# Performance work log

Measured on AMD Instinct MI355X. Metric: run time of the kernel, lower is better.

## Reference

```python
import jax
jax.config.update("jax_enable_x64", True)
import jax.numpy as jnp
import numpy as np

N = 20000      # nodes per batched graph
E = 320000     # random edges (avg degree 16)
F = 128        # input node features
EMB = 128      # embedding_size
H = 3          # num_heads
G = 128        # graphs in batch (for AvgPooling)
NEG_SLOPE = 0.2  # DGL GATConv attention LeakyReLU slope


def setup_inputs():
    key = jax.random.key(0)
    ks = jax.random.split(key, 40)

    def rn(k, shape):
        return jax.random.normal(k, shape, jnp.float32) * 0.1

    inp = {}
    inp["featsA"] = jax.random.normal(ks[0], (N, F), jnp.float32)
    inp["featsB"] = jax.random.normal(ks[1], (N, F), jnp.float32)
    # edges: random + self-loops so every node has >=1 incoming edge
    for nm, ka, kb in (("A", ks[2], ks[3]), ("B", ks[4], ks[5])):
        src = jnp.concatenate([jax.random.randint(ka, (E,), 0, N, jnp.int32),
                               jnp.arange(N, dtype=jnp.int32)])
        dst = jnp.concatenate([jax.random.randint(kb, (E,), 0, N, jnp.int32),
                               jnp.arange(N, dtype=jnp.int32)])
        inp["src" + nm] = src
        inp["dst" + nm] = dst
        inp["gid" + nm] = ((jnp.arange(N) * G) // N).astype(jnp.int32)

    # per-branch parameters (two independent GATNet_1 branches)
    i = 6
    for nm in ("A", "B"):
        inp["W1" + nm] = rn(ks[i], (F, H * EMB)); i += 1      # gat1A fc
        inp["al1" + nm] = rn(ks[i], (H, EMB)); i += 1          # attn_l
        inp["ar1" + nm] = rn(ks[i], (H, EMB)); i += 1          # attn_r
        inp["b1" + nm] = rn(ks[i], (H * EMB,)); i += 1         # bias
        inp["Wn" + nm] = rn(ks[i], (EMB, H * EMB)); i += 1     # gatn fc
        inp["aln" + nm] = rn(ks[i], (H, EMB)); i += 1
        inp["arn" + nm] = rn(ks[i], (H, EMB)); i += 1
        inp["bn" + nm] = rn(ks[i], (H * EMB,)); i += 1
        inp["Wl" + nm] = rn(ks[i], (H * EMB, EMB)); i += 1     # linear1A
        inp["bl" + nm] = rn(ks[i], (EMB,)); i += 1
    inp["Wo"] = rn(ks[i], (2 * EMB, 1)); i += 1                # DoubleNet.output
    inp["bo"] = rn(ks[i], (1,))
    return inp


def gat_layer(feat, src, dst, W, al, ar, b):
    # DGL GATConv (eval mode: feat_drop/attn_drop are identity)
    n = feat.shape[0]
    z = (feat @ W).reshape(n, H, -1)                     # [N,H,D]
    el = (z * al[None]).sum(-1)                          # [N,H]
    er = (z * ar[None]).sum(-1)
    e = jax.nn.leaky_relu(el[src] + er[dst], NEG_SLOPE)  # [E,H]
    # edge softmax over incoming edges of each dst node
    m = jax.ops.segment_max(e, dst, num_segments=n)
    a = jnp.exp(e - m[dst])
    den = jax.ops.segment_sum(a, dst, num_segments=n)
    a = a / den[dst]
    out = jax.ops.segment_sum(a[:, :, None] * z[src], dst, num_segments=n)  # [N,H,D]
    return out + b.reshape(1, H, -1)


def branch(feat, src, dst, gid, W1, al1, ar1, b1, Wn, aln, arn, bn, Wl, bl):
    n = feat.shape[0]
    x = gat_layer(feat, src, dst, W1, al1, ar1, b1).reshape(n, -1)
    x = x @ Wl + bl
    for _ in range(2):  # two applications of the SAME gatn/linear1A weights
        x = gat_layer(x, src, dst, Wn, aln, arn, bn).reshape(n, -1)
        x = x @ Wl + bl
        # nn.LeakyReLU(True): negative_slope == 1.0 -> identity (faithful)
    s = jax.ops.segment_sum(x, gid, num_segments=G)
    cnt = jax.ops.segment_sum(jnp.ones((n,), x.dtype), gid, num_segments=G)
    return s / cnt[:, None]


def reference(featsA, featsB, srcA, dstA, gidA, srcB, dstB, gidB,
              W1A, al1A, ar1A, b1A, WnA, alnA, arnA, bnA, WlA, blA,
              W1B, al1B, ar1B, b1B, WnB, alnB, arnB, bnB, WlB, blB,
              Wo, bo):
    x = branch(featsA, srcA, dstA, gidA, W1A, al1A, ar1A, b1A,
               WnA, alnA, arnA, bnA, WlA, blA)
    y = branch(featsB, srcB, dstB, gidB, W1B, al1B, ar1B, b1B,
               WnB, alnB, arnB, bnB, WlB, blB)
    cat = jnp.concatenate([x, y], axis=1)                # [G, 2*EMB]
    z = cat @ Wo + bo
    return z.astype(jnp.float64)                         # .double()
```

## Files before the change

### kernel.cpp

```cpp
#include <hip/hip_runtime.h>
#include <hip/hip_bf16.h>
#include <math.h>

#define NN  20000
#define FF  128
#define EMB 128
#define HH  3
#define GG  128
#define HD  384
#define ELL 64

typedef __attribute__((ext_vector_type(8))) short short8;
typedef __attribute__((ext_vector_type(4))) float f32x4;

__device__ inline float bf2f(unsigned int u){
  union{unsigned int i; float f;} v; v.i = u<<16; return v.f;
}
__device__ inline unsigned short f2bf(float f){
  union{unsigned int i; float f;} v; v.f = f;
  unsigned r = v.i + 0x7FFFu + ((v.i>>16)&1u);
  return (unsigned short)(r>>16);
}

__global__ __launch_bounds__(256) void prep(
    const float* __restrict__ W1A, const float* __restrict__ al1A, const float* __restrict__ ar1A,
    const float* __restrict__ WnA, const float* __restrict__ alnA, const float* __restrict__ arnA,
    const float* __restrict__ W1B, const float* __restrict__ al1B, const float* __restrict__ ar1B,
    const float* __restrict__ WnB, const float* __restrict__ alnB, const float* __restrict__ arnB,
    const float* __restrict__ WlA, const float* __restrict__ blA,
    const float* __restrict__ WlB, const float* __restrict__ blB,
    const float* __restrict__ b1A, const float* __restrict__ bnA,
    const float* __restrict__ b1B, const float* __restrict__ bnB,
    unsigned short* __restrict__ MT, float* __restrict__ V, float* __restrict__ cbuf,
    const int* __restrict__ srcA, const int* __restrict__ dstA,
    const int* __restrict__ srcB, const int* __restrict__ dstB,
    int* __restrict__ cntA, int* __restrict__ cntB,
    unsigned short* __restrict__ slotA, unsigned short* __restrict__ slotB, int ne, int nbE){
  __shared__ float As[32][65];
  __shared__ float Bs[32][65];
  int bid = blockIdx.x;
  int wv = threadIdx.x >> 6, lane = threadIdx.x & 63;

  if (bid < 48){
    int mh = bid >> 2;
    int mat = mh / 3, h = mh - mat*3;
    int tile = bid & 3; int tp = (tile>>1)*64, tq = (tile&1)*64;
    const float* W  = (mat==0)?W1A:(mat==1)?WnA:(mat==2)?W1B:WnB;
    const float* Wl = (mat<2)? WlA : WlB;
    int tid = threadIdx.x;
    int tq4 = (tid&15)<<2, tp4 = (tid>>4)<<2;
    float acc[4][4] = {};
    for (int d0=0; d0<128; d0+=32){
      {
        int p = tid>>3, dd = (tid&7)<<2;
        float4 a0 = *(const float4*)&W[(size_t)(tp+p)*HD + h*128 + d0 + dd];
        float4 a1 = *(const float4*)&W[(size_t)(tp+p+32)*HD + h*128 + d0 + dd];
        As[dd+0][p]=a0.x; As[dd+1][p]=a0.y; As[dd+2][p]=a0.z; As[dd+3][p]=a0.w;
        As[dd+0][p+32]=a1.x; As[dd+1][p+32]=a1.y; As[dd+2][p+32]=a1.z; As[dd+3][p+32]=a1.w;
      }
      {
        int dd = tid>>4, q4 = (tid&15)<<2;
        float4 b0 = *(const float4*)&Wl[(size_t)(h*128+d0+dd)*128 + tq + q4];
        float4 b1 = *(const float4*)&Wl[(size_t)(h*128+d0+dd+16)*128 + tq + q4];
        Bs[dd][q4+0]=b0.x; Bs[dd][q4+1]=b0.y; Bs[dd][q4+2]=b0.z; Bs[dd][q4+3]=b0.w;
        Bs[dd+16][q4+0]=b1.x; Bs[dd+16][q4+1]=b1.y; Bs[dd+16][q4+2]=b1.z; Bs[dd+16][q4+3]=b1.w;
      }
      __syncthreads();
      #pragma unroll
      for (int k=0;k<32;k++){
        float a[4], bb[4];
        #pragma unroll
        for (int i=0;i<4;i++) a[i] = As[k][tp4+i];
        #pragma unroll
        for (int jq=0;jq<4;jq++) bb[jq] = Bs[k][tq4+jq];
        #pragma unroll
        for (int i=0;i<4;i++)
          #pragma unroll
          for (int jq=0;jq<4;jq++)
            acc[i][jq] += a[i]*bb[jq];
      }
      __syncthreads();
    }
    #pragma unroll
    for (int jq=0;jq<4;jq++)
      #pragma unroll
      for (int i=0;i<4;i++)
        MT[(size_t)mat*49152 + (size_t)(tq+tq4+jq)*HD + h*128 + tp+tp4+i] = f2bf(acc[i][jq]);
  } else if (bid < 816){
    int idx = (bid-48)*4 + wv;
    int mat = idx / 768; int rem = idx - mat*768;
    int j = rem >> 7, k = rem & 127;
    int h = (j >= 3) ? j-3 : j; bool isr = j >= 3;
    const float* W = (mat==0)?W1A:(mat==1)?WnA:(mat==2)?W1B:WnB;
    const float* a;
    if (mat==0)      a = isr?ar1A:al1A;
    else if (mat==1) a = isr?arnA:alnA;
    else if (mat==2) a = isr?ar1B:al1B;
    else             a = isr?arnB:alnB;
    float s = W[(size_t)k*HD + h*128 + lane]      * a[h*128 + lane]
            + W[(size_t)k*HD + h*128 + 64 + lane] * a[h*128 + 64 + lane];
    #pragma unroll
    for (int o=32;o;o>>=1) s += __shfl_xor(s,o);
    if (lane == 0) V[(size_t)mat*768 + j*128 + k] = s;
  } else if (bid < 944){
    int idx = (bid-816)*4 + wv;
    int mat = idx >> 7, q = idx & 127;
    const float* bvec = (mat==0)?b1A:(mat==1)?bnA:(mat==2)?b1B:bnB;
    const float* Wl = (mat<2)?WlA:WlB;
    const float* bl = (mat<2)?blA:blB;
    float s = 0.f;
    #pragma unroll
    for (int r=0;r<6;r++){
      int j = r*64 + lane;
      s += bvec[j]*Wl[(size_t)j*128 + q];
    }
    #pragma unroll
    for (int o=32;o;o>>=1) s += __shfl_xor(s,o);
    if (lane == 0) cbuf[mat*128 + q] = s + bl[q];
  } else {
    int bb = bid - 944; int isB = bb >= nbE;
    const int* src = isB ? srcB : srcA;
    const int* dst = isB ? dstB : dstA;
    int* cnt  = isB ? cntB : cntA;
    unsigned short* slot = isB ? slotB : slotA;
    int i = (isB ? bb-nbE : bb)*256 + threadIdx.x;
    if (i < ne){
      int d = dst[i];
      int p = atomicAdd(&cnt[d], 1);
      if (p < ELL) slot[d*ELL + p] = (unsigned short)src[i];
    }
  }
}

__global__ __launch_bounds__(256) void conv_elr1(
    const float* __restrict__ fA, const float* __restrict__ fB,
    unsigned short* __restrict__ XA, unsigned short* __restrict__ XB,
    const float* __restrict__ V,
    float* __restrict__ el, float* __restrict__ er){
  int gn = blockIdx.x*4 + (threadIdx.x>>6);
  int lane = threadIdx.x & 63;
  int b = gn >= NN; int n = b ? gn - NN : gn;
  const float* feats = b ? fB : fA;
  unsigned short* X = b ? XB : XA;
  const float* Vb = V + (size_t)(b*2 + 0)*768;
  float2 xv = ((const float2*)feats)[(size_t)n*64 + lane];
  ((unsigned*)(X + (size_t)n*EMB))[lane] =
      (unsigned)f2bf(xv.x) | ((unsigned)f2bf(xv.y)<<16);
  float x0 = bf2f((unsigned)f2bf(xv.x)), x1 = bf2f((unsigned)f2bf(xv.y));
  int c0 = 2*lane;
  #pragma unroll
  for (int j=0;j<6;j++){
    float v = x0*Vb[j*128 + c0] + x1*Vb[j*128 + c0 + 1];
    #pragma unroll
    for (int o=32;o;o>>=1) v += __shfl_xor(v,o);
    if (lane == 0){
      if (j < 3) el[(size_t)gn*4 + j] = v;
      else       er[(size_t)gn*4 + (j-3)] = v;
    }
  }
}

#define GAS __attribute__((address_space(1)))
#define LAS __attribute__((address_space(3)))
__device__ inline void gll16(void* lds, const void* g){
  __builtin_amdgcn_global_load_lds((const GAS unsigned int*)g,
                                   (LAS unsigned int*)lds, 16, 0, 0);
}

__global__ __launch_bounds__(256) void gemm_mfma(
    const unsigned short* __restrict__ A0, const unsigned short* __restrict__ A1,
    const unsigned short* __restrict__ BT0, const unsigned short* __restrict__ BT1,
    const float* __restrict__ bias0, const float* __restrict__ bias1,
    unsigned short* __restrict__ C0, unsigned short* __restrict__ C1,
    int M, int N, int K){
  const unsigned short* A  = blockIdx.z ? A1 : A0;
  const unsigned short* BT = blockIdx.z ? BT1 : BT0;
  const float* bias        = blockIdx.z ? bias1 : bias0;
  unsigned short* C        = blockIdx.z ? C1 : C0;

  __shared__ __align__(16) unsigned short As[4][128][8];
  __shared__ __align__(16) unsigned short Bs[4][64][8];
  int tid = threadIdx.x;
  int w = tid >> 6, l = tid & 63;
  int wm = w >> 1, wn = w & 1;
  int l16 = l & 15, lq = l >> 4;
  int blockRow = blockIdx.y * 128;
  int blockCol = blockIdx.x * 64;
  f32x4 acc[4][2] = {};

  int arow0 = blockRow + l;       if (arow0 >= M) arow0 = M-1;
  int arow1 = blockRow + 64 + l;  if (arow1 >= M) arow1 = M-1;
  const unsigned short* aptr0 = A + (size_t)arow0*K + w*8;
  const unsigned short* aptr1 = A + (size_t)arow1*K + w*8;
  const unsigned short* bptr  = BT + (size_t)(blockCol + l)*K + w*8;
  unsigned short* alds0 = &As[w][0][0];
  unsigned short* alds1 = &As[w][64][0];
  unsigned short* blds  = &Bs[w][0][0];

  for (int k0 = 0; k0 < K; k0 += 32){
    gll16(alds0, aptr0 + k0);
    gll16(alds1, aptr1 + k0);
    gll16(blds,  bptr  + k0);
    __syncthreads();
    short8 af[4], bfr[2];
    #pragma unroll
    for (int mi=0;mi<4;mi++)
      af[mi] = *(const short8*)&As[lq][wm*64 + mi*16 + l16][0];
    #pragma unroll
    for (int ni=0;ni<2;ni++)
      bfr[ni] = *(const short8*)&Bs[lq][wn*32 + ni*16 + l16][0];
    #pragma unroll
    for (int mi=0;mi<4;mi++)
      #pragma unroll
      for (int ni=0;ni<2;ni++)
        acc[mi][ni] = __builtin_amdgcn_mfma_f32_16x16x32_bf16(af[mi], bfr[ni], acc[mi][ni], 0, 0, 0);
    __syncthreads();
  }

  #pragma unroll
  for (int ni=0;ni<2;ni++){
    int col = blockCol + wn*32 + ni*16 + l16;
    float bv = bias ? bias[col] : 0.f;
    #pragma unroll
    for (int mi=0;mi<4;mi++){
      #pragma unroll
      for (int r=0;r<4;r++){
        int row = blockRow + wm*64 + mi*16 + lq*4 + r;
        if (row < M)
          C[(size_t)row*N + col] = f2bf(acc[mi][ni][r] + bv);
      }
    }
  }
}

__global__ __launch_bounds__(256) void elr2(
    const unsigned short* __restrict__ X0, const unsigned short* __restrict__ X1,
    const float* __restrict__ V,
    float* __restrict__ el, float* __restrict__ er){
  int gn = blockIdx.x*4 + (threadIdx.x>>6);
  int lane = threadIdx.x & 63;
  int b = gn >= NN; int n = b ? gn - NN : gn;
  const unsigned short* X = b ? X1 : X0;
  const float* Vb = V + (size_t)(b*2 + 1)*768;
  unsigned u = ((const unsigned*)(X + (size_t)n*EMB))[lane];
  float xlo = bf2f(u & 0xFFFFu), xhi = bf2f(u>>16);
  int c0 = 2*lane;
  #pragma unroll
  for (int j=0;j<6;j++){
    float v = xlo*Vb[j*128 + c0] + xhi*Vb[j*128 + c0 + 1];
    #pragma unroll
    for (int o=32;o;o>>=1) v += __shfl_xor(v,o);
    if (lane == 0){
      if (j < 3) el[(size_t)gn*4 + j] = v;
      else       er[(size_t)gn*4 + (j-3)] = v;
    }
  }
}

__global__ __launch_bounds__(256) void gat_agg(
    const unsigned short* __restrict__ X0, const unsigned short* __restrict__ X1,
    const float* __restrict__ el, const float* __restrict__ er,
    const int* __restrict__ cntA, const int* __restrict__ cntB,
    const unsigned short* __restrict__ slotA, const unsigned short* __restrict__ slotB,
    unsigned short* __restrict__ U0, unsigned short* __restrict__ U1){
  int wv = threadIdx.x >> 6, lane = threadIdx.x & 63;
  int gn = blockIdx.x*4 + wv;
  int b = gn >= NN; int n = b ? gn - NN : gn;
  const unsigned short* X = b ? X1 : X0;
  const int* cnt  = b ? cntB : cntA;
  const unsigned short* slot = b ? slotB : slotA;
  unsigned short* U = b ? U1 : U0;
  const float* elb = el + (size_t)b*NN*4;

  int deg = cnt[n]; if (deg > ELL) deg = ELL;
  float er0 = er[(size_t)gn*4+0], er1 = er[(size_t)gn*4+1], er2 = er[(size_t)gn*4+2];

  int s = 0;
  float e0 = -3e38f, e1 = -3e38f, e2 = -3e38f;
  if (lane < deg){
    s = (int)slot[n*ELL + lane];
    float4 ev = *(const float4*)(elb + (size_t)s*4);
    float t0 = ev.x+er0; e0 = t0>0.f ? t0 : 0.2f*t0;
    float t1 = ev.y+er1; e1 = t1>0.f ? t1 : 0.2f*t1;
    float t2 = ev.z+er2; e2 = t2>0.f ? t2 : 0.2f*t2;
  }
  float m0 = e0, m1 = e1, m2 = e2;
  #pragma unroll
  for (int o=32;o;o>>=1){
    m0 = fmaxf(m0, __shfl_xor(m0,o));
    m1 = fmaxf(m1, __shfl_xor(m1,o));
    m2 = fmaxf(m2, __shfl_xor(m2,o));
  }
  float p0 = __expf(e0-m0), p1 = __expf(e1-m1), p2 = __expf(e2-m2);
  float d0 = p0, d1 = p1, d2 = p2;
  #pragma unroll
  for (int o=32;o;o>>=1){
    d0 += __shfl_xor(d0,o); d1 += __shfl_xor(d1,o); d2 += __shfl_xor(d2,o);
  }
  float a0 = p0/d0, a1 = p1/d1, a2 = p2/d2;
  int a0i = __float_as_int(a0), a1i = __float_as_int(a1), a2i = __float_as_int(a2);

  float ax0=0.f,ay0=0.f,ax1=0.f,ay1=0.f,ax2=0.f,ay2=0.f;
  const unsigned* Xw = (const unsigned*)X;
  int npad = (deg + 3) & ~3;
  for (int e = 0; e < npad; e += 4){
    #pragma unroll
    for (int u2 = 0; u2 < 4; u2++){
      int idx = e + u2;
      int sl = __builtin_amdgcn_readlane(s, idx);
      float w0 = __int_as_float(__builtin_amdgcn_readlane(a0i, idx));
      float w1 = __int_as_float(__builtin_amdgcn_readlane(a1i, idx));
      float w2 = __int_as_float(__builtin_amdgcn_readlane(a2i, idx));
      unsigned xu = Xw[(size_t)sl*64 + lane];
      float lo = __int_as_float(xu << 16);
      float hi = __int_as_float(xu & 0xffff0000u);
      ax0 += w0*lo; ay0 += w0*hi;
      ax1 += w1*lo; ay1 += w1*hi;
      ax2 += w2*lo; ay2 += w2*hi;
    }
  }

  unsigned* op = (unsigned*)(U + (size_t)n*HD);
  op[lane]      = (unsigned)f2bf(ax0) | ((unsigned)f2bf(ay0)<<16);
  op[64+lane]   = (unsigned)f2bf(ax1) | ((unsigned)f2bf(ay1)<<16);
  op[128+lane]  = (unsigned)f2bf(ax2) | ((unsigned)f2bf(ay2)<<16);
}

__device__ inline int lbound(const int* __restrict__ a, int n, int v){
  int lo = 0, hi = n;
  while (lo < hi){ int mid = (lo+hi)>>1; if (a[mid] < v) lo = mid+1; else hi = mid; }
  return lo;
}

__global__ __launch_bounds__(512) void pool_kernel(
    const unsigned short* __restrict__ X0, const unsigned short* __restrict__ X1,
    const int* __restrict__ gidA, const int* __restrict__ gidB,
    float* __restrict__ ps){
  int bg = blockIdx.x;
  int b = bg >= GG; int g = b ? bg-GG : bg;
  const unsigned short* X = b ? X1 : X0;
  const int* gid = b ? gidB : gidA;
  int lo = lbound(gid, NN, g), hi = lbound(gid, NN, g+1);
  int t = threadIdx.x;
  int rl = t >> 6, c2 = t & 63;
  float ax = 0.f, ay = 0.f;
  for (int n = lo + rl; n < hi; n += 8){
    unsigned u = ((const unsigned*)(X + (size_t)n*EMB))[c2];
    ax += bf2f(u & 0xFFFFu); ay += bf2f(u >> 16);
  }
  __shared__ float sh[8][128];
  sh[rl][2*c2] = ax; sh[rl][2*c2+1] = ay;
  __syncthreads();
  if (t < 128){
    float s = 0.f;
    #pragma unroll
    for (int r=0;r<8;r++) s += sh[r][t];
    ps[(size_t)bg*EMB + t] = s / (float)(hi - lo);
  }
}

__global__ void final_kernel(const float* __restrict__ ps,
                             const float* __restrict__ Wo, const float* __restrict__ bo,
                             float* __restrict__ out){
  int g = blockIdx.x*4 + (threadIdx.x>>6);
  int lane = threadIdx.x & 63;
  if (g >= GG) return;
  float v = 0.f;
  #pragma unroll
  for (int r=0;r<4;r++){
    int k = r*64 + lane;
    float cv = (k < EMB) ? ps[(size_t)g*EMB + k]
                         : ps[(size_t)(GG + g)*EMB + (k-EMB)];
    v += cv * Wo[k];
  }
  #pragma unroll
  for (int o=32;o;o>>=1) v += __shfl_xor(v,o);
  if (lane == 0) out[g] = v + bo[0];
}

extern "C" void kernel_launch(void* const* d_in, const int* in_sizes, int n_in,
                              void* d_out, int out_size, void* d_ws, size_t ws_size,
                              hipStream_t stream){
  const float* featsA = (const float*)d_in[0];
  const float* featsB = (const float*)d_in[1];
  const int* srcA = (const int*)d_in[2];
  const int* dstA = (const int*)d_in[3];
  const int* gidA = (const int*)d_in[4];
  const int* srcB = (const int*)d_in[5];
  const int* dstB = (const int*)d_in[6];
  const int* gidB = (const int*)d_in[7];
  const int EE = in_sizes[2];
  const float* P[2][10];
  for (int b=0;b<2;b++)
    for (int j=0;j<10;j++)
      P[b][j] = (const float*)d_in[8 + b*10 + j];
  const float* Wo = (const float*)d_in[28];
  const float* bo = (const float*)d_in[29];
  float* out = (float*)d_out;

  char* ws = (char*)d_ws;
  size_t o = 0;
  auto alloc = [&](size_t bytes)->char*{
    char* p = ws + o; o += (bytes + 255) & ~(size_t)255; return p;
  };
  unsigned short* bufU[2] = {(unsigned short*)alloc((size_t)NN*HD*2),
                             (unsigned short*)alloc((size_t)NN*HD*2)};
  unsigned short* bufX[2] = {(unsigned short*)alloc((size_t)NN*EMB*2),
                             (unsigned short*)alloc((size_t)NN*EMB*2)};
  unsigned short* fbf[2] = {(unsigned short*)alloc((size_t)NN*FF*2),
                            (unsigned short*)alloc((size_t)NN*FF*2)};
  unsigned short* MT = (unsigned short*)alloc((size_t)4*49152*2);
  float* V    = (float*)alloc((size_t)4*768*4);
  float* cbuf = (float*)alloc((size_t)4*128*4);
  float* el   = (float*)alloc((size_t)2*NN*4*4);
  float* er   = (float*)alloc((size_t)2*NN*4*4);
  int*   cntA = (int*)alloc((size_t)2*NN*4);
  int*   cntB = cntA + NN;
  unsigned short* slotA = (unsigned short*)alloc((size_t)NN*ELL*2);
  unsigned short* slotB = (unsigned short*)alloc((size_t)NN*ELL*2);
  float* ps   = (float*)alloc((size_t)2*GG*EMB*4);

  const int nbE = (EE + 255)/256;
  const int nwB = 2*NN/4;
  dim3 gWL(EMB/64, (NN+127)/128, 2);

  hipMemsetAsync(cntA, 0, (size_t)2*NN*4, stream);
  prep<<<944 + 2*nbE, 256, 0, stream>>>(
      P[0][0],P[0][1],P[0][2], P[0][4],P[0][5],P[0][6],
      P[1][0],P[1][1],P[1][2], P[1][4],P[1][5],P[1][6],
      P[0][8],P[0][9], P[1][8],P[1][9],
      P[0][3],P[0][7], P[1][3],P[1][7],
      MT, V, cbuf,
      srcA,dstA, srcB,dstB, cntA,cntB, slotA,slotB, EE, nbE);
  conv_elr1<<<nwB,256,0,stream>>>(featsA, featsB, fbf[0], fbf[1], V, el, er);

  gat_agg<<<nwB,256,0,stream>>>(fbf[0], fbf[1], el, er, cntA,cntB, slotA,slotB,
                                bufU[0], bufU[1]);
  gemm_mfma<<<gWL,256,0,stream>>>(bufU[0],bufU[1], MT + 0*49152, MT + 2*49152,
                                  cbuf + 0*128, cbuf + 2*128,
                                  bufX[0],bufX[1], NN, EMB, HD);

  for (int it=0; it<2; it++){
    elr2<<<nwB,256,0,stream>>>(bufX[0], bufX[1], V, el, er);
    gat_agg<<<nwB,256,0,stream>>>(bufX[0], bufX[1], el, er, cntA,cntB, slotA,slotB,
                                  bufU[0], bufU[1]);
    gemm_mfma<<<gWL,256,0,stream>>>(bufU[0],bufU[1], MT + 1*49152, MT + 3*49152,
                                    cbuf + 1*128, cbuf + 3*128,
                                    bufX[0],bufX[1], NN, EMB, HD);
  }

  pool_kernel<<<2*GG,512,0,stream>>>(bufX[0],bufX[1], gidA,gidB, ps);
  final_kernel<<<(GG+3)/4,256,0,stream>>>(ps, Wo, bo, out);
}
```

Baseline: 291.8 us.

## Fuse GAT aggregation, projection GEMM and attention-score computation into one layer kernel

Replaces the separate gat_agg, gemm_mfma and elr2 kernels with one layer_fused kernel. Each block aggregates 16 nodes into LDS, runs the 384x128 projection with MFMA straight from LDS, adds the bias, writes the bf16 output, and computes the next layer's el/er from the output via shuffle reductions. This removes the 384-wide intermediate U buffer round trip through global memory and two launches per layer. In exchange, neighbor slots are widened to int, the weight tile is read from global by every block with no LDS reuse, and the per-block MFMA work is small, so GEMM efficiency may drop.

```diff
diff --git a/kernel.cpp b/kernel.cpp
--- a/kernel.cpp
+++ b/kernel.cpp
@@ -35,7 +35,7 @@
     const int* __restrict__ srcA, const int* __restrict__ dstA,
     const int* __restrict__ srcB, const int* __restrict__ dstB,
     int* __restrict__ cntA, int* __restrict__ cntB,
-    unsigned short* __restrict__ slotA, unsigned short* __restrict__ slotB, int ne, int nbE){
+    int* __restrict__ slotA, int* __restrict__ slotB, int ne, int nbE){
   __shared__ float As[32][65];
   __shared__ float Bs[32][65];
   int bid = blockIdx.x;
@@ -122,12 +122,12 @@
     const int* src = isB ? srcB : srcA;
     const int* dst = isB ? dstB : dstA;
     int* cnt  = isB ? cntB : cntA;
-    unsigned short* slot = isB ? slotB : slotA;
+    int* slot = isB ? slotB : slotA;
     int i = (isB ? bb-nbE : bb)*256 + threadIdx.x;
     if (i < ne){
       int d = dst[i];
       int p = atomicAdd(&cnt[d], 1);
-      if (p < ELL) slot[d*ELL + p] = (unsigned short)src[i];
+      if (p < ELL) slot[d*ELL + p] = src[i];
     }
   }
 }
@@ -160,170 +160,145 @@
   }
 }
 
-#define GAS __attribute__((address_space(1)))
-#define LAS __attribute__((address_space(3)))
-__device__ inline void gll16(void* lds, const void* g){
-  __builtin_amdgcn_global_load_lds((const GAS unsigned int*)g,
-                                   (LAS unsigned int*)lds, 16, 0, 0);
-}
-
-__global__ __launch_bounds__(256) void gemm_mfma(
-    const unsigned short* __restrict__ A0, const unsigned short* __restrict__ A1,
-    const unsigned short* __restrict__ BT0, const unsigned short* __restrict__ BT1,
-    const float* __restrict__ bias0, const float* __restrict__ bias1,
-    unsigned short* __restrict__ C0, unsigned short* __restrict__ C1,
-    int M, int N, int K){
-  const unsigned short* A  = blockIdx.z ? A1 : A0;
-  const unsigned short* BT = blockIdx.z ? BT1 : BT0;
-  const float* bias        = blockIdx.z ? bias1 : bias0;
-  unsigned short* C        = blockIdx.z ? C1 : C0;
-
-  __shared__ __align__(16) unsigned short As[4][128][8];
-  __shared__ __align__(16) unsigned short Bs[4][64][8];
-  int tid = threadIdx.x;
-  int w = tid >> 6, l = tid & 63;
-  int wm = w >> 1, wn = w & 1;
-  int l16 = l & 15, lq = l >> 4;
-  int blockRow = blockIdx.y * 128;
-  int blockCol = blockIdx.x * 64;
-  f32x4 acc[4][2] = {};
-
-  int arow0 = blockRow + l;       if (arow0 >= M) arow0 = M-1;
-  int arow1 = blockRow + 64 + l;  if (arow1 >= M) arow1 = M-1;
-  const unsigned short* aptr0 = A + (size_t)arow0*K + w*8;
-  const unsigned short* aptr1 = A + (size_t)arow1*K + w*8;
-  const unsigned short* bptr  = BT + (size_t)(blockCol + l)*K + w*8;
-  unsigned short* alds0 = &As[w][0][0];
-  unsigned short* alds1 = &As[w][64][0];
-  unsigned short* blds  = &Bs[w][0][0];
-
-  for (int k0 = 0; k0 < K; k0 += 32){
-    gll16(alds0, aptr0 + k0);
-    gll16(alds1, aptr1 + k0);
-    gll16(blds,  bptr  + k0);
-    __syncthreads();
-    short8 af[4], bfr[2];
-    #pragma unroll
-    for (int mi=0;mi<4;mi++)
-      af[mi] = *(const short8*)&As[lq][wm*64 + mi*16 + l16][0];
-    #pragma unroll
-    for (int ni=0;ni<2;ni++)
-      bfr[ni] = *(const short8*)&Bs[lq][wn*32 + ni*16 + l16][0];
-    #pragma unroll
-    for (int mi=0;mi<4;mi++)
-      #pragma unroll
-      for (int ni=0;ni<2;ni++)
-        acc[mi][ni] = __builtin_amdgcn_mfma_f32_16x16x32_bf16(af[mi], bfr[ni], acc[mi][ni], 0, 0, 0);
-    __syncthreads();
-  }
-
-  #pragma unroll
-  for (int ni=0;ni<2;ni++){
-    int col = blockCol + wn*32 + ni*16 + l16;
-    float bv = bias ? bias[col] : 0.f;
-    #pragma unroll
-    for (int mi=0;mi<4;mi++){
-      #pragma unroll
-      for (int r=0;r<4;r++){
-        int row = blockRow + wm*64 + mi*16 + lq*4 + r;
-        if (row < M)
-          C[(size_t)row*N + col] = f2bf(acc[mi][ni][r] + bv);
-      }
-    }
-  }
-}
-
-__global__ __launch_bounds__(256) void elr2(
-    const unsigned short* __restrict__ X0, const unsigned short* __restrict__ X1,
-    const float* __restrict__ V,
-    float* __restrict__ el, float* __restrict__ er){
-  int gn = blockIdx.x*4 + (threadIdx.x>>6);
-  int lane = threadIdx.x & 63;
-  int b = gn >= NN; int n = b ? gn - NN : gn;
-  const unsigned short* X = b ? X1 : X0;
-  const float* Vb = V + (size_t)(b*2 + 1)*768;
-  unsigned u = ((const unsigned*)(X + (size_t)n*EMB))[lane];
-  float xlo = bf2f(u & 0xFFFFu), xhi = bf2f(u>>16);
-  int c0 = 2*lane;
-  #pragma unroll
-  for (int j=0;j<6;j++){
-    float v = xlo*Vb[j*128 + c0] + xhi*Vb[j*128 + c0 + 1];
-    #pragma unroll
-    for (int o=32;o;o>>=1) v += __shfl_xor(v,o);
-    if (lane == 0){
-      if (j < 3) el[(size_t)gn*4 + j] = v;
-      else       er[(size_t)gn*4 + (j-3)] = v;
-    }
-  }
-}
-
-__global__ __launch_bounds__(256) void gat_agg(
+__global__ __launch_bounds__(256) void layer_fused(
     const unsigned short* __restrict__ X0, const unsigned short* __restrict__ X1,
     const float* __restrict__ el, const float* __restrict__ er,
     const int* __restrict__ cntA, const int* __restrict__ cntB,
-    const unsigned short* __restrict__ slotA, const unsigned short* __restrict__ slotB,
-    unsigned short* __restrict__ U0, unsigned short* __restrict__ U1){
+    const int* __restrict__ slotA, const int* __restrict__ slotB,
+    const unsigned short* __restrict__ MT_A, const unsigned short* __restrict__ MT_B,
+    const float* __restrict__ cb_A, const float* __restrict__ cb_B,
+    const float* __restrict__ V, int vsel,
+    float* __restrict__ elN, float* __restrict__ erN,
+    unsigned short* __restrict__ Xo0, unsigned short* __restrict__ Xo1){
+  __shared__ unsigned short Ul[16][392];
+  __shared__ float part[4][16][6];
   int wv = threadIdx.x >> 6, lane = threadIdx.x & 63;
-  int gn = blockIdx.x*4 + wv;
-  int b = gn >= NN; int n = b ? gn - NN : gn;
+  int bid = blockIdx.x;
+  int b = bid >= (NN/16);
+  int base = (b ? bid - NN/16 : bid) * 16;
   const unsigned short* X = b ? X1 : X0;
   const int* cnt  = b ? cntB : cntA;
-  const unsigned short* slot = b ? slotB : slotA;
-  unsigned short* U = b ? U1 : U0;
+  const int* slot = b ? slotB : slotA;
   const float* elb = el + (size_t)b*NN*4;
-
-  int deg = cnt[n]; if (deg > ELL) deg = ELL;
-  float er0 = er[(size_t)gn*4+0], er1 = er[(size_t)gn*4+1], er2 = er[(size_t)gn*4+2];
-
-  int s = 0;
-  float e0 = -3e38f, e1 = -3e38f, e2 = -3e38f;
-  if (lane < deg){
-    s = (int)slot[n*ELL + lane];
-    float4 ev = *(const float4*)(elb + (size_t)s*4);
-    float t0 = ev.x+er0; e0 = t0>0.f ? t0 : 0.2f*t0;
-    float t1 = ev.y+er1; e1 = t1>0.f ? t1 : 0.2f*t1;
-    float t2 = ev.z+er2; e2 = t2>0.f ? t2 : 0.2f*t2;
-  }
-  float m0 = e0, m1 = e1, m2 = e2;
+  const float* erb = er + (size_t)b*NN*4;
+
+  const unsigned* Xw = (const unsigned*)X;
+  for (int i = 0; i < 4; i++){
+    int nloc = wv*4 + i;
+    int n = base + nloc;
+    int deg = cnt[n]; if (deg > ELL) deg = ELL;
+    float er0 = erb[(size_t)n*4+0], er1 = erb[(size_t)n*4+1], er2 = erb[(size_t)n*4+2];
+
+    int s = 0;
+    float e0 = -3e38f, e1 = -3e38f, e2 = -3e38f;
+    if (lane < deg){
+      s = slot[n*ELL + lane];
+      float4 ev = *(const float4*)(elb + (size_t)s*4);
+      float t0 = ev.x+er0; e0 = t0>0.f ? t0 : 0.2f*t0;
+      float t1 = ev.y+er1; e1 = t1>0.f ? t1 : 0.2f*t1;
+      float t2 = ev.z+er2; e2 = t2>0.f ? t2 : 0.2f*t2;
+    }
+    float m0 = e0, m1 = e1, m2 = e2;
+    #pragma unroll
+    for (int o=32;o;o>>=1){
+      m0 = fmaxf(m0, __shfl_xor(m0,o));
+      m1 = fmaxf(m1, __shfl_xor(m1,o));
+      m2 = fmaxf(m2, __shfl_xor(m2,o));
+    }
+    float p0 = __expf(e0-m0), p1 = __expf(e1-m1), p2 = __expf(e2-m2);
+    float d0 = p0, d1 = p1, d2 = p2;
+    #pragma unroll
+    for (int o=32;o;o>>=1){
+      d0 += __shfl_xor(d0,o); d1 += __shfl_xor(d1,o); d2 += __shfl_xor(d2,o);
+    }
+    float a0 = p0/d0, a1 = p1/d1, a2 = p2/d2;
+    int a0i = __float_as_int(a0), a1i = __float_as_int(a1), a2i = __float_as_int(a2);
+
+    float ax0=0.f,ay0=0.f,ax1=0.f,ay1=0.f,ax2=0.f,ay2=0.f;
+    int npad = (deg + 3) & ~3;
+    for (int e = 0; e < npad; e += 4){
+      #pragma unroll
+      for (int u2 = 0; u2 < 4; u2++){
+        int idx = e + u2;
+        int sl = __builtin_amdgcn_readlane(s, idx);
+        float w0 = __int_as_float(__builtin_amdgcn_readlane(a0i, idx));
+        float w1 = __int_as_float(__builtin_amdgcn_readlane(a1i, idx));
+        float w2 = __int_as_float(__builtin_amdgcn_readlane(a2i, idx));
+        unsigned xu = Xw[(size_t)sl*64 + lane];
+        float lo = __int_as_float(xu << 16);
+        float hi = __int_as_float(xu & 0xffff0000u);
+        ax0 += w0*lo; ay0 += w0*hi;
+        ax1 += w1*lo; ay1 += w1*hi;
+        ax2 += w2*lo; ay2 += w2*hi;
+      }
+    }
+    unsigned* urow = (unsigned*)&Ul[nloc][0];
+    urow[lane]      = (unsigned)f2bf(ax0) | ((unsigned)f2bf(ay0)<<16);
+    urow[64+lane]   = (unsigned)f2bf(ax1) | ((unsigned)f2bf(ay1)<<16);
+    urow[128+lane]  = (unsigned)f2bf(ax2) | ((unsigned)f2bf(ay2)<<16);
+  }
+  __syncthreads();
+
+  int l16 = lane & 15, lq = lane >> 4;
+  const unsigned short* MTb = b ? MT_B : MT_A;
+  int col0 = wv*32 + l16;
+  int col1 = col0 + 16;
+  const unsigned short* bp0 = MTb + (size_t)col0*HD + lq*8;
+  const unsigned short* bp1 = MTb + (size_t)col1*HD + lq*8;
+  f32x4 acc0 = {0.f,0.f,0.f,0.f}, acc1 = {0.f,0.f,0.f,0.f};
   #pragma unroll
-  for (int o=32;o;o>>=1){
-    m0 = fmaxf(m0, __shfl_xor(m0,o));
-    m1 = fmaxf(m1, __shfl_xor(m1,o));
-    m2 = fmaxf(m2, __shfl_xor(m2,o));
-  }
-  float p0 = __expf(e0-m0), p1 = __expf(e1-m1), p2 = __expf(e2-m2);
-  float d0 = p0, d1 = p1, d2 = p2;
+  for (int k0 = 0; k0 < HD; k0 += 32){
+    short8 af = *(const short8*)&Ul[l16][k0 + lq*8];
+    short8 b0 = *(const short8*)&bp0[k0];
+    short8 b1 = *(const short8*)&bp1[k0];
+    acc0 = __builtin_amdgcn_mfma_f32_16x16x32_bf16(af, b0, acc0, 0, 0, 0);
+    acc1 = __builtin_amdgcn_mfma_f32_16x16x32_bf16(af, b1, acc1, 0, 0, 0);
+  }
+
+  const float* cbb = b ? cb_B : cb_A;
+  unsigned short* Xout = b ? Xo1 : Xo0;
+  float cv0 = cbb[col0], cv1 = cbb[col1];
+  float vv0[6], vv1[6];
+  if (vsel >= 0){
+    const float* Vv = V + (size_t)(b*2 + vsel)*768;
+    #pragma unroll
+    for (int j=0;j<6;j++){ vv0[j] = Vv[j*128 + col0]; vv1[j] = Vv[j*128 + col1]; }
+  }
   #pragma unroll
-  for (int o=32;o;o>>=1){
-    d0 += __shfl_xor(d0,o); d1 += __shfl_xor(d1,o); d2 += __shfl_xor(d2,o);
-  }
-  float a0 = p0/d0, a1 = p1/d1, a2 = p2/d2;
-  int a0i = __float_as_int(a0), a1i = __float_as_int(a1), a2i = __float_as_int(a2);
-
-  float ax0=0.f,ay0=0.f,ax1=0.f,ay1=0.f,ax2=0.f,ay2=0.f;
-  const unsigned* Xw = (const unsigned*)X;
-  int npad = (deg + 3) & ~3;
-  for (int e = 0; e < npad; e += 4){
-    #pragma unroll
-    for (int u2 = 0; u2 < 4; u2++){
-      int idx = e + u2;
-      int sl = __builtin_amdgcn_readlane(s, idx);
-      float w0 = __int_as_float(__builtin_amdgcn_readlane(a0i, idx));
-      float w1 = __int_as_float(__builtin_amdgcn_readlane(a1i, idx));
-      float w2 = __int_as_float(__builtin_amdgcn_readlane(a2i, idx));
-      unsigned xu = Xw[(size_t)sl*64 + lane];
-      float lo = __int_as_float(xu << 16);
-      float hi = __int_as_float(xu & 0xffff0000u);
-      ax0 += w0*lo; ay0 += w0*hi;
-      ax1 += w1*lo; ay1 += w1*hi;
-      ax2 += w2*lo; ay2 += w2*hi;
-    }
-  }
-
-  unsigned* op = (unsigned*)(U + (size_t)n*HD);
-  op[lane]      = (unsigned)f2bf(ax0) | ((unsigned)f2bf(ay0)<<16);
-  op[64+lane]   = (unsigned)f2bf(ax1) | ((unsigned)f2bf(ay1)<<16);
-  op[128+lane]  = (unsigned)f2bf(ax2) | ((unsigned)f2bf(ay2)<<16);
+  for (int r = 0; r < 4; r++){
+    int nloc = lq*4 + r;
+    int n = base + nloc;
+    float x0 = acc0[r] + cv0, x1 = acc1[r] + cv1;
+    unsigned short xb0 = f2bf(x0), xb1 = f2bf(x1);
+    Xout[(size_t)n*EMB + col0] = xb0;
+    Xout[(size_t)n*EMB + col1] = xb1;
+    if (vsel >= 0){
+      float xr0 = bf2f(xb0), xr1 = bf2f(xb1);
+      float p[6];
+      #pragma unroll
+      for (int j=0;j<6;j++) p[j] = xr0*vv0[j] + xr1*vv1[j];
+      #pragma unroll
+      for (int j=0;j<6;j++){
+        #pragma unroll
+        for (int o=1;o<16;o<<=1) p[j] += __shfl_xor(p[j], o);
+      }
+      if (l16 == 0){
+        #pragma unroll
+        for (int j=0;j<6;j++) part[wv][nloc][j] = p[j];
+      }
+    }
+  }
+  if (vsel >= 0){
+    __syncthreads();
+    int t = threadIdx.x;
+    if (t < 96){
+      int nloc = t / 6, j = t - (t/6)*6;
+      float s2 = part[0][nloc][j] + part[1][nloc][j] + part[2][nloc][j] + part[3][nloc][j];
+      size_t gn = (size_t)b*NN + base + nloc;
+      if (j < 3) elN[gn*4 + j] = s2;
+      else       erN[gn*4 + (j-3)] = s2;
+    }
+  }
 }
 
 __device__ inline int lbound(const int* __restrict__ a, int n, int v){
@@ -403,26 +378,30 @@
   auto alloc = [&](size_t bytes)->char*{
     char* p = ws + o; o += (bytes + 255) & ~(size_t)255; return p;
   };
-  unsigned short* bufU[2] = {(unsigned short*)alloc((size_t)NN*HD*2),
-                             (unsigned short*)alloc((size_t)NN*HD*2)};
-  unsigned short* bufX[2] = {(unsigned short*)alloc((size_t)NN*EMB*2),
-                             (unsigned short*)alloc((size_t)NN*EMB*2)};
   unsigned short* fbf[2] = {(unsigned short*)alloc((size_t)NN*FF*2),
                             (unsigned short*)alloc((size_t)NN*FF*2)};
+  unsigned short* Xa[2] = {(unsigned short*)alloc((size_t)NN*EMB*2),
+                           (unsigned short*)alloc((size_t)NN*EMB*2)};
+  unsigned short* Xb[2] = {(unsigned short*)alloc((size_t)NN*EMB*2),
+                           (unsigned short*)alloc((size_t)NN*EMB*2)};
   unsigned short* MT = (unsigned short*)alloc((size_t)4*49152*2);
   float* V    = (float*)alloc((size_t)4*768*4);
   float* cbuf = (float*)alloc((size_t)4*128*4);
-  float* el   = (float*)alloc((size_t)2*NN*4*4);
-  float* er   = (float*)alloc((size_t)2*NN*4*4);
+  float* el0  = (float*)alloc((size_t)2*NN*4*4);
+  float* er0  = (float*)alloc((size_t)2*NN*4*4);
+  float* el1  = (float*)alloc((size_t)2*NN*4*4);
+  float* er1  = (float*)alloc((size_t)2*NN*4*4);
+  float* el2  = (float*)alloc((size_t)2*NN*4*4);
+  float* er2  = (float*)alloc((size_t)2*NN*4*4);
   int*   cntA = (int*)alloc((size_t)2*NN*4);
   int*   cntB = cntA + NN;
-  unsigned short* slotA = (unsigned short*)alloc((size_t)NN*ELL*2);
-  unsigned short* slotB = (unsigned short*)alloc((size_t)NN*ELL*2);
+  int*   slotA= (int*)alloc((size_t)NN*ELL*4);
+  int*   slotB= (int*)alloc((size_t)NN*ELL*4);
   float* ps   = (float*)alloc((size_t)2*GG*EMB*4);
 
   const int nbE = (EE + 255)/256;
   const int nwB = 2*NN/4;
-  dim3 gWL(EMB/64, (NN+127)/128, 2);
+  const int nLB = 2*NN/16;
 
   hipMemsetAsync(cntA, 0, (size_t)2*NN*4, stream);
   prep<<<944 + 2*nbE, 256, 0, stream>>>(
@@ -432,23 +411,21 @@
       P[0][3],P[0][7], P[1][3],P[1][7],
       MT, V, cbuf,
       srcA,dstA, srcB,dstB, cntA,cntB, slotA,slotB, EE, nbE);
-  conv_elr1<<<nwB,256,0,stream>>>(featsA, featsB, fbf[0], fbf[1], V, el, er);
-
-  gat_agg<<<nwB,256,0,stream>>>(fbf[0], fbf[1], el, er, cntA,cntB, slotA,slotB,
-                                bufU[0], bufU[1]);
-  gemm_mfma<<<gWL,256,0,stream>>>(bufU[0],bufU[1], MT + 0*49152, MT + 2*49152,
-                                  cbuf + 0*128, cbuf + 2*128,
-                                  bufX[0],bufX[1], NN, EMB, HD);
-
-  for (int it=0; it<2; it++){
-    elr2<<<nwB,256,0,stream>>>(bufX[0], bufX[1], V, el, er);
-    gat_agg<<<nwB,256,0,stream>>>(bufX[0], bufX[1], el, er, cntA,cntB, slotA,slotB,
-                                  bufU[0], bufU[1]);
-    gemm_mfma<<<gWL,256,0,stream>>>(bufU[0],bufU[1], MT + 1*49152, MT + 3*49152,
+  conv_elr1<<<nwB,256,0,stream>>>(featsA, featsB, fbf[0], fbf[1], V, el0, er0);
+
+  layer_fused<<<nLB,256,0,stream>>>(fbf[0], fbf[1], el0, er0, cntA,cntB, slotA,slotB,
+                                    MT + 0*49152, MT + 2*49152,
+                                    cbuf + 0*128, cbuf + 2*128,
+                                    V, 1, el1, er1, Xa[0], Xa[1]);
+  layer_fused<<<nLB,256,0,stream>>>(Xa[0], Xa[1], el1, er1, cntA,cntB, slotA,slotB,
+                                    MT + 1*49152, MT + 3*49152,
                                     cbuf + 1*128, cbuf + 3*128,
-                                    bufX[0],bufX[1], NN, EMB, HD);
-  }
-
-  pool_kernel<<<2*GG,512,0,stream>>>(bufX[0],bufX[1], gidA,gidB, ps);
+                                    V, 1, el2, er2, Xb[0], Xb[1]);
+  layer_fused<<<nLB,256,0,stream>>>(Xb[0], Xb[1], el2, er2, cntA,cntB, slotA,slotB,
+                                    MT + 1*49152, MT + 3*49152,
+                                    cbuf + 1*128, cbuf + 3*128,
+                                    V, -1, nullptr, nullptr, Xa[0], Xa[1]);
+
+  pool_kernel<<<2*GG,512,0,stream>>>(Xa[0],Xa[1], gidA,gidB, ps);
   final_kernel<<<(GG+3)/4,256,0,stream>>>(ps, Wo, bo, out);
 }
```

Measured after the change: 268.1 us. 8.1% less time.
